# Kernel tuning notes

Measured on AMD Instinct MI355X. Metric: run time of the kernel, lower is better.

Reference implementation:

```python
import jax, jax.numpy as jnp
import numpy as np

EPS_BN = 1e-5
EPS_LN = 1e-5

def _gelu(x):
    return jax.nn.gelu(x, approximate=False)  # torch nn.GELU default is erf-based

def _conv(x, w, b, stride):
    y = jax.lax.conv_general_dilated(x, w, (stride, stride), 'VALID',
                                     dimension_numbers=('NCHW', 'OIHW', 'NCHW'))
    return y + b[None, :, None, None]

def _bn_train(x, g, b):
    # training-mode BatchNorm2d: batch statistics over (N,H,W), biased variance
    m = x.mean(axis=(0, 2, 3), keepdims=True)
    v = ((x - m) ** 2).mean(axis=(0, 2, 3), keepdims=True)
    return g[None, :, None, None] * (x - m) * jax.lax.rsqrt(v + EPS_BN) + b[None, :, None, None]

def _ln(x, g, b):
    m = x.mean(-1, keepdims=True)
    v = ((x - m) ** 2).mean(-1, keepdims=True)
    return g * (x - m) * jax.lax.rsqrt(v + EPS_LN) + b

def setup_inputs() -> dict:
    key = jax.random.key(0)
    ks = jax.random.split(key, 16)
    B, E, D, H = 1024, 8, 256, 512
    cnn_out = 128 * 14 * 16  # 28672
    s = 0.02
    inp = {
        'x': jax.random.normal(ks[0], (B, 4, 144, 160), jnp.float32),
        'conv1_w': jax.random.normal(ks[1], (32, 4, 8, 8), jnp.float32) * s,
        'conv1_b': jnp.zeros((32,), jnp.float32),
        'bn1_g': jnp.ones((32,), jnp.float32), 'bn1_b': jnp.zeros((32,), jnp.float32),
        'conv2_w': jax.random.normal(ks[2], (64, 32, 4, 4), jnp.float32) * s,
        'conv2_b': jnp.zeros((64,), jnp.float32),
        'bn2_g': jnp.ones((64,), jnp.float32), 'bn2_b': jnp.zeros((64,), jnp.float32),
        'conv3_w': jax.random.normal(ks[3], (128, 64, 3, 3), jnp.float32) * s,
        'conv3_b': jnp.zeros((128,), jnp.float32),
        'bn3_g': jnp.ones((128,), jnp.float32), 'bn3_b': jnp.zeros((128,), jnp.float32),
        'proj_w': jax.random.normal(ks[4], (D, cnn_out), jnp.float32) * 0.005,
        'proj_b': jnp.zeros((D,), jnp.float32),
        'ln_g': jnp.ones((D,), jnp.float32), 'ln_b': jnp.zeros((D,), jnp.float32),
        'router_w': jax.random.normal(ks[5], (E, D), jnp.float32) * 0.01,
        'expert_bias': jnp.zeros((E,), jnp.float32),
        'ew1': jax.random.normal(ks[6], (E, H, D), jnp.float32) * s,
        'eb1': jnp.zeros((E, H), jnp.float32),
        'ew2': jax.random.normal(ks[7], (E, D, H), jnp.float32) * s,
        'eb2': jnp.zeros((E, D), jnp.float32),
        'sw1': jax.random.normal(ks[8], (D, D), jnp.float32) * s,  # shared expert hidden = 512//2 = 256
        'sb1': jnp.zeros((D,), jnp.float32),
        'sw2': jax.random.normal(ks[9], (D, D), jnp.float32) * s,
        'sb2': jnp.zeros((D,), jnp.float32),
        'moe_ln_g': jnp.ones((D,), jnp.float32), 'moe_ln_b': jnp.zeros((D,), jnp.float32),
    }
    return inp

def reference(x, conv1_w, conv1_b, bn1_g, bn1_b, conv2_w, conv2_b, bn2_g, bn2_b,
              conv3_w, conv3_b, bn3_g, bn3_b, proj_w, proj_b, ln_g, ln_b,
              router_w, expert_bias, ew1, eb1, ew2, eb2, sw1, sb1, sw2, sb2,
              moe_ln_g, moe_ln_b):
    B = x.shape[0]
    E = router_w.shape[0]
    top_k = 2
    # conv backbone
    h = _gelu(_bn_train(_conv(x, conv1_w, conv1_b, 4), bn1_g, bn1_b))
    h = _gelu(_bn_train(_conv(h, conv2_w, conv2_b, 2), bn2_g, bn2_b))
    h = _gelu(_bn_train(_conv(h, conv3_w, conv3_b, 1), bn3_g, bn3_b))
    h = h.reshape(B, -1)  # [B, 128*14*16]
    # projection
    h = _gelu(_ln(h @ proj_w.T + proj_b, ln_g, ln_b))  # [B, 256]
    # router (eval: no noise)
    logits = h @ router_w.T + expert_bias          # [B, E]
    probs = jax.nn.softmax(logits, axis=-1)
    wts, idx = jax.lax.top_k(probs, top_k)          # [B, k]
    wts = wts / (wts.sum(-1, keepdims=True) + 1e-8)
    # dense expert compute, sparse combine (same math as masked dispatch loop)
    hid = _gelu(jnp.einsum('bd,ehd->beh', h, ew1) + eb1)   # [B, E, 512]
    eout = jnp.einsum('beh,edh->bed', hid, ew2) + eb2       # [B, E, 256]
    combine = jnp.zeros((B, E), h.dtype).at[jnp.arange(B)[:, None], idx].add(wts)
    out = jnp.einsum('be,bed->bd', combine, eout)
    # shared expert
    shared = _gelu(h @ sw1.T + sb1) @ sw2.T + sb2
    out = out + 0.5 * shared
    # aux losses
    pm = probs.mean(0)
    lb_loss = ((pm - 1.0 / E) ** 2).sum() * E
    z_loss = (logits ** 2).mean() * 0.001
    out = _ln(out, moe_ln_g, moe_ln_b)
    return out, lb_loss, z_loss
```

## Files before the change

kernel.cpp:

```cpp
#include <hip/hip_runtime.h>
#include <hip/hip_bf16.h>
#include <math.h>

typedef unsigned short u16;
typedef unsigned int u32;
typedef __attribute__((ext_vector_type(8))) short bf16x8;
typedef __attribute__((ext_vector_type(4))) float f32x4;

#define DEV __device__ __forceinline__

DEV float gelu_f(float x) { return 0.5f * x * (1.0f + erff(x * 0.70710678118654752f)); }
DEV u16 f2bf(float f) { u32 u = __builtin_bit_cast(u32, f); u = (u + 0x7FFFu + ((u >> 16) & 1u)) >> 16; return (u16)u; }
DEV float bf2f(u16 h) { return __builtin_bit_cast(float, (u32)h << 16); }
DEV u32 fbits(float f) { return __builtin_bit_cast(u32, f); }
DEV float ubits(u32 u) { return __builtin_bit_cast(float, u); }
DEV u32 psplit(float v) {
  u32 u = fbits(v);
  float lo = v - ubits(u & 0xFFFF0000u);
  return (u >> 16) | (fbits(lo) & 0xFFFF0000u);
}
DEV float punp(u32 p) { return ubits(p << 16) + ubits(p & 0xFFFF0000u); }
DEV f32x4 mfma3(bf16x8 ah, bf16x8 al, bf16x8 bh, bf16x8 bl, f32x4 c) {
  c = __builtin_amdgcn_mfma_f32_16x16x32_bf16(al, bh, c, 0, 0, 0);
  c = __builtin_amdgcn_mfma_f32_16x16x32_bf16(ah, bl, c, 0, 0, 0);
  c = __builtin_amdgcn_mfma_f32_16x16x32_bf16(ah, bh, c, 0, 0, 0);
  return c;
}

__global__ void k_zero(float* p, int n) {
  int i = blockIdx.x * blockDim.x + threadIdx.x;
  if (i < n) p[i] = 0.f;
}

__global__ void k_wprep1(const float* __restrict__ w, u16* __restrict__ wh, u16* __restrict__ wl) {
  int idx = blockIdx.x * 256 + threadIdx.x; if (idx >= 8192) return;
  int j = idx & 7, lane = (idx >> 3) & 63, s = (idx >> 9) & 7, oct = idx >> 12;
  int oc = oct * 16 + (lane & 15);
  int kl = ((lane >> 4) << 3) + j;
  int kw = kl >> 2, c = kl & 3, kh = s;
  float v = w[((oc * 4 + c) * 8 + kh) * 8 + kw];
  u16 h = f2bf(v); wh[idx] = h; wl[idx] = f2bf(v - bf2f(h));
}
__global__ void k_wprep2(const float* __restrict__ w, u16* __restrict__ wh, u16* __restrict__ wl) {
  int idx = blockIdx.x * 256 + threadIdx.x; if (idx >= 32768) return;
  int j = idx & 7, lane = (idx >> 3) & 63, s = (idx >> 9) & 15, oct = idx >> 13;
  int oc = oct * 16 + (lane & 15);
  int k = s * 32 + ((lane >> 4) << 3) + j;
  int kh = k >> 7, kw = (k >> 5) & 3, c = k & 31;
  float v = w[((oc * 32 + c) * 4 + kh) * 4 + kw];
  u16 h = f2bf(v); wh[idx] = h; wl[idx] = f2bf(v - bf2f(h));
}
__global__ void k_wprep3(const float* __restrict__ w, u16* __restrict__ wh, u16* __restrict__ wl) {
  int idx = blockIdx.x * 256 + threadIdx.x; if (idx >= 73728) return;
  int j = idx & 7, lane = (idx >> 3) & 63, rest = idx >> 9;
  int s = rest % 18, oct = rest / 18;
  int oc = oct * 16 + (lane & 15);
  int k = s * 32 + ((lane >> 4) << 3) + j;
  int kh = k / 192, r = k - kh * 192;
  int kw = r >> 6, c = r & 63;
  float v = w[((oc * 64 + c) * 3 + kh) * 3 + kw];
  u16 h = f2bf(v); wh[idx] = h; wl[idx] = f2bf(v - bf2f(h));
}
__global__ __launch_bounds__(256) void k_wprepP(const float* __restrict__ w,
    u16* __restrict__ wh, u16* __restrict__ wl)
{
  __shared__ float tile[16][4][225];
  int q = blockIdx.x, oct = blockIdx.y, tid = threadIdx.x;
  for (int i = tid; i < 3584; i += 256) {
    int n = i / 224, rem = i % 224, e = rem / 56, f4 = rem % 56;
    float4 v = *(const float4*)(w + (long)(oct * 16 + n) * 28672 + (4 * q + e) * 224 + f4 * 4);
    tile[n][e][f4 * 4 + 0] = v.x; tile[n][e][f4 * 4 + 1] = v.y;
    tile[n][e][f4 * 4 + 2] = v.z; tile[n][e][f4 * 4 + 3] = v.w;
  }
  __syncthreads();
  int g = (q >> 1) & 3, j0 = 4 * (q & 1), sgb = q >> 3;
  for (int o = tid; o < 3584; o += 256) {
    int pix = o >> 4, ln = o & 15;
    u16 hs[4], ls[4];
#pragma unroll
    for (int e = 0; e < 4; ++e) {
      float v = tile[ln][e][pix];
      u16 h = f2bf(v); hs[e] = h; ls[e] = f2bf(v - bf2f(h));
    }
    long base = (((long)oct * 896 + pix * 4 + sgb) * 64 + g * 16 + ln) * 8 + j0;
    *(uint2*)(wh + base) = make_uint2((u32)hs[0] | ((u32)hs[1] << 16), (u32)hs[2] | ((u32)hs[3] << 16));
    *(uint2*)(wl + base) = make_uint2((u32)ls[0] | ((u32)ls[1] << 16), (u32)ls[2] | ((u32)ls[3] << 16));
  }
}
__global__ void k_wprepG(const float* __restrict__ w, u16* __restrict__ wf,
                         int N, int K, long total)
{
  long idx = (long)blockIdx.x * 256 + threadIdx.x; if (idx >= total) return;
  int j = (int)(idx & 7); int lane = (int)((idx >> 3) & 63); long rest = idx >> 9;
  int kn = K >> 5;
  int s = (int)(rest % kn); long rest2 = rest / kn;
  int noct = N >> 4;
  int oct = (int)(rest2 % noct); int z = (int)(rest2 / noct);
  int n = oct * 16 + (lane & 15);
  int k = s * 32 + ((lane >> 4) << 3) + j;
  wf[idx] = f2bf(w[((long)z * N + n) * K + k]);
}

__global__ __launch_bounds__(256, 3) void k_conv1m(const float* __restrict__ x,
    const u16* __restrict__ wfh, const u16* __restrict__ wfl,
    const float* __restrict__ bias, u32* __restrict__ y1p, float* __restrict__ sums)
{
  __shared__ __align__(16) u16 sin0[12800], sin1[12800];
  __shared__ float bs1[32], bs2[32];
  int ohp = blockIdx.x, b = blockIdx.y, tid = threadIdx.x;
  int row0 = ohp * 16;
  if (tid < 32) { bs1[tid] = 0.f; bs2[tid] = 0.f; }
  for (int i = tid; i < 1600; i += 256) {
    int cp = i / 800, rem = i - cp * 800, r = rem / 40, q = rem - r * 40;
    int grow = row0 + r;
    float4 v0 = make_float4(0.f, 0.f, 0.f, 0.f), v1 = v0;
    if (grow < 144) {
      long base = ((long)b * 4 + 2 * cp) * 23040 + (long)grow * 160 + q * 4;
      v0 = *(const float4*)(x + base);
      v1 = *(const float4*)(x + base + 23040);
    }
    const float* a0 = (const float*)&v0;
    const float* a1 = (const float*)&v1;
#pragma unroll
    for (int m = 0; m < 4; ++m) {
      float f0 = a0[m], f1 = a1[m];
      u32 u0 = fbits(f0), u1 = fbits(f1);
      u32 hh = (u0 >> 16) | (u1 & 0xFFFF0000u);
      float l0 = f0 - ubits(u0 & 0xFFFF0000u);
      float l1 = f1 - ubits(u1 & 0xFFFF0000u);
      u32 ll = (fbits(l0) >> 16) | (fbits(l1) & 0xFFFF0000u);
      int col = q * 4 + m;
      int idx = r * 320 + col * 2 + cp;
      idx ^= ((col >> 4) & 3) << 2;
      ((u32*)sin0)[idx] = hh;
      ((u32*)sin1)[idx] = ll;
    }
  }
  __syncthreads();
  int w = tid >> 6, lane = tid & 63, g = lane >> 4, ln = lane & 15;
  int ohls[3], owcs[3];
#pragma unroll
  for (int jj = 0; jj < 3; ++jj) {
    int j = w + 4 * jj;
    ohls[jj] = j / 3;
    int owc = (j % 3) * 16 + ln; if (owc > 38) owc = 38;
    owcs[jj] = owc;
  }
  f32x4 z4 = {0.f, 0.f, 0.f, 0.f};
  f32x4 acc[3][2];
#pragma unroll
  for (int jj = 0; jj < 3; ++jj) { acc[jj][0] = z4; acc[jj][1] = z4; }
#pragma unroll
  for (int kh = 0; kh < 8; ++kh) {
    bf16x8 bh0 = *(const bf16x8*)&wfh[kh * 512 + lane * 8];
    bf16x8 bl0 = *(const bf16x8*)&wfl[kh * 512 + lane * 8];
    bf16x8 bh1 = *(const bf16x8*)&wfh[4096 + kh * 512 + lane * 8];
    bf16x8 bl1 = *(const bf16x8*)&wfl[4096 + kh * 512 + lane * 8];
#pragma unroll
    for (int jj = 0; jj < 3; ++jj) {
      int col = owcs[jj] * 4 + g * 2;
      int off = (4 * ohls[jj] + kh) * 640 + col * 4;
      off ^= ((col >> 4) & 3) << 3;
      bf16x8 ah = *(const bf16x8*)&sin0[off];
      bf16x8 al = *(const bf16x8*)&sin1[off];
      acc[jj][0] = mfma3(ah, al, bh0, bl0, acc[jj][0]);
      acc[jj][1] = mfma3(ah, al, bh1, bl1, acc[jj][1]);
    }
  }
  float s1[2] = {0.f, 0.f}, s2[2] = {0.f, 0.f};
#pragma unroll
  for (int jj = 0; jj < 3; ++jj) {
    int j = w + 4 * jj;
    int ohl = j / 3, owt = j % 3;
    int oh = 4 * ohp + ohl;
    if (oh >= 35) continue;
#pragma unroll
    for (int oct = 0; oct < 2; ++oct) {
      int oc = oct * 16 + ln;
      float bv = bias[oc];
#pragma unroll
      for (int r = 0; r < 4; ++r) {
        int owo = owt * 16 + g * 4 + r;
        if (owo < 39) {
          long oi = ((long)b * 1365 + oh * 39 + owo) * 32 + oc;
          float v = acc[jj][oct][r] + bv;
          y1p[oi] = psplit(v);
          s1[oct] += v; s2[oct] += v * v;
        }
      }
    }
  }
#pragma unroll
  for (int o = 16; o <= 32; o <<= 1) {
    s1[0] += __shfl_xor(s1[0], o); s1[1] += __shfl_xor(s1[1], o);
    s2[0] += __shfl_xor(s2[0], o); s2[1] += __shfl_xor(s2[1], o);
  }
  if (g == 0) {
    atomicAdd(&bs1[ln], s1[0]); atomicAdd(&bs1[16 + ln], s1[1]);
    atomicAdd(&bs2[ln], s2[0]); atomicAdd(&bs2[16 + ln], s2[1]);
  }
  __syncthreads();
  if (tid < 32) {
    atomicAdd(&sums[tid], bs1[tid]);
    atomicAdd(&sums[32 + tid], bs2[tid]);
  }
}

__global__ __launch_bounds__(256, 3) void k_conv2m(const u32* __restrict__ y1p,
    const u16* __restrict__ wfh, const u16* __restrict__ wfl,
    const float* __restrict__ scale, const float* __restrict__ shift,
    const float* __restrict__ bias, u32* __restrict__ y2p, float* __restrict__ sums)
{
  __shared__ __align__(16) u16 sin0[12480], sin1[12480];
  __shared__ float sc[32], shf[32];
  __shared__ float bs1[64], bs2[64];
  int ohq = blockIdx.x, b = blockIdx.y, tid = threadIdx.x;
  if (tid < 32) { sc[tid] = scale[tid]; shf[tid] = shift[tid]; }
  if (tid < 64) { bs1[tid] = 0.f; bs2[tid] = 0.f; }
  __syncthreads();
  long sb = ((long)b * 1365 + (long)ohq * 312) * 32;
  const uint4* srcP = (const uint4*)(y1p + sb);
  for (int i = tid; i < 3120; i += 256) {
    uint4 p4 = srcP[i];
    int cb = (i & 7) * 4;
    u32 hw[2], lw[2];
    u32 pe[4] = { p4.x, p4.y, p4.z, p4.w };
#pragma unroll
    for (int half = 0; half < 2; ++half) {
      float va = punp(pe[half * 2 + 0]);
      float vb = punp(pe[half * 2 + 1]);
      float aa = gelu_f(va * sc[cb + half * 2 + 0] + shf[cb + half * 2 + 0]);
      float ab = gelu_f(vb * sc[cb + half * 2 + 1] + shf[cb + half * 2 + 1]);
      u32 ua = fbits(aa), ub = fbits(ab);
      float la = aa - ubits(ua & 0xFFFF0000u);
      float lb = ab - ubits(ub & 0xFFFF0000u);
      hw[half] = (ua >> 16) | (ub & 0xFFFF0000u);
      lw[half] = (fbits(la) >> 16) | (fbits(lb) & 0xFFFF0000u);
    }
    int iw = i ^ (((i >> 4) & 7) << 1);
    ((uint2*)sin0)[iw] = make_uint2(hw[0], hw[1]);
    ((uint2*)sin1)[iw] = make_uint2(lw[0], lw[1]);
  }
  __syncthreads();
  int w = tid >> 6, lane = tid & 63, g = lane >> 4, ln = lane & 15;
  int oct = w;
  int rowb[5], colb[5];
#pragma unroll
  for (int j = 0; j < 5; ++j) {
    int p = j * 16 + ln; if (p > 71) p = 71;
    int ohl = p / 18, ow = p - 18 * ohl;
    rowb[j] = 2 * ohl; colb[j] = 2 * ow;
  }
  f32x4 z4 = {0.f, 0.f, 0.f, 0.f};
  f32x4 acc[5];
#pragma unroll
  for (int j = 0; j < 5; ++j) acc[j] = z4;
#pragma unroll
  for (int s = 0; s < 16; ++s) {
    int kh = s >> 2, kw = s & 3;
    bf16x8 bh = *(const bf16x8*)&wfh[oct * 8192 + s * 512 + lane * 8];
    bf16x8 bl = *(const bf16x8*)&wfl[oct * 8192 + s * 512 + lane * 8];
#pragma unroll
    for (int j = 0; j < 5; ++j) {
      int colpix = (rowb[j] + kh) * 39 + colb[j] + kw;
      int off = colpix * 32 + g * 8;
      off ^= ((colpix >> 1) & 7) << 3;
      bf16x8 ah = *(const bf16x8*)&sin0[off];
      bf16x8 al = *(const bf16x8*)&sin1[off];
      acc[j] = mfma3(ah, al, bh, bl, acc[j]);
    }
  }
  int oc = oct * 16 + ln;
  float bv = bias[oc];
  float s1 = 0.f, s2 = 0.f;
#pragma unroll
  for (int j = 0; j < 5; ++j) {
#pragma unroll
    for (int r = 0; r < 4; ++r) {
      int po = j * 16 + g * 4 + r;
      if (po < 72) {
        long oi = ((long)b * 288 + (long)ohq * 72 + po) * 64 + oc;
        float v = acc[j][r] + bv;
        y2p[oi] = psplit(v);
        s1 += v; s2 += v * v;
      }
    }
  }
#pragma unroll
  for (int o = 16; o <= 32; o <<= 1) { s1 += __shfl_xor(s1, o); s2 += __shfl_xor(s2, o); }
  if (g == 0) { atomicAdd(&bs1[oc], s1); atomicAdd(&bs2[oc], s2); }
  __syncthreads();
  if (tid < 64) {
    atomicAdd(&sums[tid], bs1[tid]);
    atomicAdd(&sums[64 + tid], bs2[tid]);
  }
}

__global__ __launch_bounds__(256, 3) void k_conv3m(const u32* __restrict__ y2p,
    const u16* __restrict__ wfh, const u16* __restrict__ wfl,
    const float* __restrict__ scale, const float* __restrict__ shift,
    const float* __restrict__ bias, u32* __restrict__ y3p, float* __restrict__ sums)
{
  __shared__ __align__(16) u16 sin0[10368], sin1[10368];
  __shared__ float sc[64], shf[64];
  __shared__ float bs1[128], bs2[128];
  int hh = blockIdx.x, b = blockIdx.y, tid = threadIdx.x;
  if (tid < 64) { sc[tid] = scale[tid]; shf[tid] = shift[tid]; }
  if (tid < 128) { bs1[tid] = 0.f; bs2[tid] = 0.f; }
  __syncthreads();
  long sb = ((long)b * 288 + (long)hh * 126) * 64;
  const uint4* srcP = (const uint4*)(y2p + sb);
  for (int i = tid; i < 2592; i += 256) {
    uint4 p4 = srcP[i];
    int cb = (i & 15) * 4;
    u32 hw[2], lw[2];
    u32 pe[4] = { p4.x, p4.y, p4.z, p4.w };
#pragma unroll
    for (int half = 0; half < 2; ++half) {
      float va = punp(pe[half * 2 + 0]);
      float vb = punp(pe[half * 2 + 1]);
      float aa = gelu_f(va * sc[cb + half * 2 + 0] + shf[cb + half * 2 + 0]);
      float ab = gelu_f(vb * sc[cb + half * 2 + 1] + shf[cb + half * 2 + 1]);
      u32 ua = fbits(aa), ub = fbits(ab);
      float la = aa - ubits(ua & 0xFFFF0000u);
      float lb = ab - ubits(ub & 0xFFFF0000u);
      hw[half] = (ua >> 16) | (ub & 0xFFFF0000u);
      lw[half] = (fbits(la) >> 16) | (fbits(lb) & 0xFFFF0000u);
    }
    int iw = i ^ (((i >> 4) & 7) << 1);
    ((uint2*)sin0)[iw] = make_uint2(hw[0], hw[1]);
    ((uint2*)sin1)[iw] = make_uint2(lw[0], lw[1]);
  }
  __syncthreads();
  int w = tid >> 6, lane = tid & 63, g = lane >> 4, ln = lane & 15;
  int oct0 = w * 2;
  f32x4 z4 = {0.f, 0.f, 0.f, 0.f};
  f32x4 acc[7][2];
#pragma unroll
  for (int j = 0; j < 7; ++j) { acc[j][0] = z4; acc[j][1] = z4; }
#pragma unroll 6
  for (int s = 0; s < 18; ++s) {
    const int kh = s / 6, rm = s % 6;
    const int kw = rm >> 1, ch = rm & 1;
    bf16x8 bh0 = *(const bf16x8*)&wfh[oct0 * 9216 + s * 512 + lane * 8];
    bf16x8 bl0 = *(const bf16x8*)&wfl[oct0 * 9216 + s * 512 + lane * 8];
    bf16x8 bh1 = *(const bf16x8*)&wfh[(oct0 + 1) * 9216 + s * 512 + lane * 8];
    bf16x8 bl1 = *(const bf16x8*)&wfl[(oct0 + 1) * 9216 + s * 512 + lane * 8];
#pragma unroll
    for (int j = 0; j < 7; ++j) {
      int colpix = (j + kh) * 18 + ln + kw;
      int off = colpix * 64 + ch * 32 + g * 8;
      off ^= (colpix & 7) << 3;
      bf16x8 ah = *(const bf16x8*)&sin0[off];
      bf16x8 al = *(const bf16x8*)&sin1[off];
      acc[j][0] = mfma3(ah, al, bh0, bl0, acc[j][0]);
      acc[j][1] = mfma3(ah, al, bh1, bl1, acc[j][1]);
    }
  }
  float s1[2] = {0.f, 0.f}, s2[2] = {0.f, 0.f};
#pragma unroll
  for (int j = 0; j < 7; ++j) {
#pragma unroll
    for (int o2 = 0; o2 < 2; ++o2) {
      int oc = (oct0 + o2) * 16 + ln;
      float bv = bias[oc];
#pragma unroll
      for (int r = 0; r < 4; ++r) {
        int owo = g * 4 + r;
        long oi = ((long)b * 224 + (hh * 7 + j) * 16 + owo) * 128 + oc;
        float v = acc[j][o2][r] + bv;
        y3p[oi] = psplit(v);
        s1[o2] += v; s2[o2] += v * v;
      }
    }
  }
#pragma unroll
  for (int o = 16; o <= 32; o <<= 1) {
    s1[0] += __shfl_xor(s1[0], o); s1[1] += __shfl_xor(s1[1], o);
    s2[0] += __shfl_xor(s2[0], o); s2[1] += __shfl_xor(s2[1], o);
  }
  if (g == 0) {
    atomicAdd(&bs1[oct0 * 16 + ln], s1[0]); atomicAdd(&bs1[(oct0 + 1) * 16 + ln], s1[1]);
    atomicAdd(&bs2[oct0 * 16 + ln], s2[0]); atomicAdd(&bs2[(oct0 + 1) * 16 + ln], s2[1]);
  }
  __syncthreads();
  if (tid < 128) {
    atomicAdd(&sums[tid], bs1[tid]);
    atomicAdd(&sums[128 + tid], bs2[tid]);
  }
}

__global__ void k_bn_finalize(const float* __restrict__ sums, const float* __restrict__ g,
    const float* __restrict__ b, float* __restrict__ scale, float* __restrict__ shift,
    int C, float invN)
{
  int c = threadIdx.x;
  if (c < C) {
    float m = sums[c] * invN;
    float var = sums[C + c] * invN - m * m;
    float sc = g[c] * rsqrtf(var + 1e-5f);
    scale[c] = sc;
    shift[c] = b[c] - m * sc;
  }
}

__global__ __launch_bounds__(256, 2) void k_projm(const u32* __restrict__ y3p,
    const u16* __restrict__ bh_g, const u16* __restrict__ bl_g,
    const float* __restrict__ scale, const float* __restrict__ shift,
    float* __restrict__ part)
{
  __shared__ __align__(16) u16 Ah[2048], Al[2048];
  __shared__ __align__(16) u16 Bh[8192], Bl[8192];
  __shared__ float sc3[128], sh3[128];
  int m0 = blockIdx.x * 64, by = blockIdx.y, tid = threadIdx.x;
  int w = tid >> 6, lane = tid & 63, g = lane >> 4, ln = lane & 15;
  if (tid < 128) { sc3[tid] = scale[tid]; sh3[tid] = shift[tid]; }
  f32x4 z4 = {0.f, 0.f, 0.f, 0.f};
  f32x4 acc[16];
#pragma unroll
  for (int o = 0; o < 16; ++o) acc[o] = z4;
  for (int ks = 0; ks < 28; ++ks) {
    __syncthreads();
    long k0 = ((long)by * 28 + ks) * 32;
    int cbase = (int)(k0 & 127);
    {
      for (int ii = 0; ii < 2; ++ii) {
        int i = tid + ii * 256;
        int row = i >> 3, q = i & 7;
        uint4 p4 = *((const uint4*)(y3p + (long)(m0 + row) * 28672 + k0) + q);
        u32 pe[4] = { p4.x, p4.y, p4.z, p4.w };
        int c0 = cbase + q * 4;
        u16 hs[4], ls[4];
#pragma unroll
        for (int j = 0; j < 4; ++j) {
          float v = punp(pe[j]);
          float a = gelu_f(v * sc3[c0 + j] + sh3[c0 + j]);
          u32 ua = fbits(a);
          float la = a - ubits(ua & 0xFFFF0000u);
          hs[j] = (u16)(ua >> 16);
          ls[j] = (u16)(fbits(la) >> 16);
        }
        ((uint2*)Ah)[i] = make_uint2((u32)hs[0] | ((u32)hs[1] << 16), (u32)hs[2] | ((u32)hs[3] << 16));
        ((uint2*)Al)[i] = make_uint2((u32)ls[0] | ((u32)ls[1] << 16), (u32)ls[2] | ((u32)ls[3] << 16));
      }
    }
    int ksg = by * 28 + ks;
#pragma unroll
    for (int ii = 0; ii < 8; ++ii) {
      int i = tid + ii * 256;
      int arr = i >> 10, idx = i & 1023, oct = idx >> 6, r2 = idx & 63;
      const u16* src = arr ? bl_g : bh_g;
      u16* dst = arr ? Bl : Bh;
      ((uint4*)dst)[idx] = *((const uint4*)(src + ((long)oct * 896 + ksg) * 512) + r2);
    }
    __syncthreads();
    bf16x8 a_h = *(const bf16x8*)&Ah[(w * 16 + ln) * 32 + g * 8];
    bf16x8 a_l = *(const bf16x8*)&Al[(w * 16 + ln) * 32 + g * 8];
#pragma unroll
    for (int oct = 0; oct < 16; ++oct) {
      bf16x8 bh = *(const bf16x8*)&Bh[oct * 512 + lane * 8];
      bf16x8 bl = *(const bf16x8*)&Bl[oct * 512 + lane * 8];
      acc[oct] = mfma3(a_h, a_l, bh, bl, acc[oct]);
    }
  }
#pragma unroll
  for (int oct = 0; oct < 16; ++oct) {
    int oc = oct * 16 + ln;
#pragma unroll
    for (int r = 0; r < 4; ++r) {
      int tok = m0 + w * 16 + g * 4 + r;
      part[((long)by * 1024 + tok) * 256 + oc] = acc[oct][r];
    }
  }
}

__global__ __launch_bounds__(256) void k_lnred(const float* __restrict__ part,
    const float* __restrict__ pb, const float* __restrict__ g, const float* __restrict__ be,
    float* __restrict__ h, u16* __restrict__ hb)
{
  int b = blockIdx.x, d = threadIdx.x;
  float s = pb[d];
#pragma unroll
  for (int ks = 0; ks < 32; ++ks) s += part[((long)ks * 1024 + b) * 256 + d];
  __shared__ float red[4];
  float t = s;
  for (int o = 32; o; o >>= 1) t += __shfl_xor(t, o);
  if ((d & 63) == 0) red[d >> 6] = t;
  __syncthreads();
  float mean = (red[0] + red[1] + red[2] + red[3]) * (1.f / 256.f);
  __syncthreads();
  float dv = s - mean;
  t = dv * dv;
  for (int o = 32; o; o >>= 1) t += __shfl_xor(t, o);
  if ((d & 63) == 0) red[d >> 6] = t;
  __syncthreads();
  float var = (red[0] + red[1] + red[2] + red[3]) * (1.f / 256.f);
  float hv = gelu_f(g[d] * dv * rsqrtf(var + 1e-5f) + be[d]);
  h[b * 256 + d] = hv;
  hb[b * 256 + d] = f2bf(hv);
}

__global__ __launch_bounds__(256, 2) void k_gemmb(const u16* __restrict__ A, long aZ, int K,
    const u16* __restrict__ Bf, int noct_tot,
    const float* __restrict__ bias, int biasZ,
    void* __restrict__ C, long cZ, int ldc, int outbf, int act)
{
  __shared__ __align__(16) u16 As[2048];
  __shared__ __align__(16) u16 Bs[8192];
  int m0 = blockIdx.x * 64, nb = blockIdx.y, z = blockIdx.z, tid = threadIdx.x;
  int w = tid >> 6, lane = tid & 63, g = lane >> 4, ln = lane & 15;
  const u16* Az = A + (long)z * aZ;
  int kn = K >> 5;
  f32x4 z4 = {0.f, 0.f, 0.f, 0.f};
  f32x4 acc[16];
#pragma unroll
  for (int o = 0; o < 16; ++o) acc[o] = z4;
  for (int ks = 0; ks < kn; ++ks) {
    __syncthreads();
    {
      int row = tid >> 2, q = tid & 3;
      ((uint4*)As)[tid] = *((const uint4*)(Az + (long)(m0 + row) * K + ks * 32) + q);
    }
#pragma unroll
    for (int ii = 0; ii < 4; ++ii) {
      int i = tid + ii * 256;
      int oct = i >> 6, r2 = i & 63;
      const u16* src = Bf + (((long)z * noct_tot + nb * 16 + oct) * kn + ks) * 512;
      ((uint4*)Bs)[i] = ((const uint4*)src)[r2];
    }
    __syncthreads();
    bf16x8 a = *(const bf16x8*)&As[(w * 16 + ln) * 32 + g * 8];
#pragma unroll
    for (int oct = 0; oct < 16; ++oct) {
      bf16x8 bb = *(const bf16x8*)&Bs[oct * 512 + lane * 8];
      acc[oct] = __builtin_amdgcn_mfma_f32_16x16x32_bf16(a, bb, acc[oct], 0, 0, 0);
    }
  }
#pragma unroll
  for (int oct = 0; oct < 16; ++oct) {
    int n = nb * 256 + oct * 16 + ln;
    float bv = bias[z * biasZ + n];
#pragma unroll
    for (int r = 0; r < 4; ++r) {
      int tok = m0 + w * 16 + g * 4 + r;
      float v = acc[oct][r] + bv;
      if (act) v = gelu_f(v);
      long off = (long)z * cZ + (long)tok * ldc + n;
      if (outbf) ((u16*)C)[off] = f2bf(v);
      else ((float*)C)[off] = v;
    }
  }
}

__global__ __launch_bounds__(64) void k_router(const float* __restrict__ h,
    const float* __restrict__ rw, const float* __restrict__ eb,
    float* __restrict__ wts, int* __restrict__ idx,
    float* __restrict__ pm_sum, float* __restrict__ z_sum)
{
  int b = blockIdx.x, lane = threadIdx.x;
  float4 hv = *(const float4*)(h + b * 256 + lane * 4);
  float logit[8];
#pragma unroll
  for (int e = 0; e < 8; ++e) {
    float4 wv = *(const float4*)(rw + e * 256 + lane * 4);
    float p = hv.x * wv.x + hv.y * wv.y + hv.z * wv.z + hv.w * wv.w;
    for (int o = 32; o; o >>= 1) p += __shfl_xor(p, o);
    logit[e] = p + eb[e];
  }
  float mx = logit[0];
#pragma unroll
  for (int e = 1; e < 8; ++e) mx = fmaxf(mx, logit[e]);
  float pr[8]; float se = 0.f;
#pragma unroll
  for (int e = 0; e < 8; ++e) { pr[e] = expf(logit[e] - mx); se += pr[e]; }
  float inv = 1.f / se;
#pragma unroll
  for (int e = 0; e < 8; ++e) pr[e] *= inv;
  int i0 = 0; float v0 = pr[0];
#pragma unroll
  for (int e = 1; e < 8; ++e) if (pr[e] > v0) { v0 = pr[e]; i0 = e; }
  int i1 = -1; float v1 = -1.f;
#pragma unroll
  for (int e = 0; e < 8; ++e) if (e != i0 && pr[e] > v1) { v1 = pr[e]; i1 = e; }
  if (lane == 0) {
    float ssum = v0 + v1 + 1e-8f;
    wts[2 * b] = v0 / ssum; wts[2 * b + 1] = v1 / ssum;
    idx[2 * b] = i0; idx[2 * b + 1] = i1;
    float zz = 0.f;
#pragma unroll
    for (int e = 0; e < 8; ++e) zz += logit[e] * logit[e];
    atomicAdd(z_sum, zz);
  }
  if (lane < 8) atomicAdd(&pm_sum[lane], pr[lane]);
}

__global__ __launch_bounds__(256) void k_combine_ln(const float* __restrict__ eout,
    const float* __restrict__ sharedB, const float* __restrict__ wts, const int* __restrict__ idx,
    const float* __restrict__ g, const float* __restrict__ bb, float* __restrict__ out)
{
  int b = blockIdx.x, d = threadIdx.x;
  float w0 = wts[2 * b], w1 = wts[2 * b + 1];
  int i0 = idx[2 * b], i1 = idx[2 * b + 1];
  float val = w0 * eout[(long)i0 * 262144 + b * 256 + d]
            + w1 * eout[(long)i1 * 262144 + b * 256 + d]
            + 0.5f * sharedB[b * 256 + d];
  __shared__ float red[4];
  float s = val;
  for (int o = 32; o; o >>= 1) s += __shfl_xor(s, o);
  if ((d & 63) == 0) red[d >> 6] = s;
  __syncthreads();
  float mean = (red[0] + red[1] + red[2] + red[3]) * (1.f / 256.f);
  __syncthreads();
  float dv = val - mean;
  s = dv * dv;
  for (int o = 32; o; o >>= 1) s += __shfl_xor(s, o);
  if ((d & 63) == 0) red[d >> 6] = s;
  __syncthreads();
  float var = (red[0] + red[1] + red[2] + red[3]) * (1.f / 256.f);
  out[b * 256 + d] = g[d] * dv * rsqrtf(var + 1e-5f) + bb[d];
}

__global__ void k_losses(const float* __restrict__ pm_sum, const float* __restrict__ z_sum,
                         float* __restrict__ out)
{
  if (threadIdx.x == 0 && blockIdx.x == 0) {
    float lb = 0.f;
    for (int e = 0; e < 8; ++e) {
      float pm = pm_sum[e] * (1.f / 1024.f);
      float dd = pm - 0.125f;
      lb += dd * dd;
    }
    out[262144] = lb * 8.f;
    out[262145] = z_sum[0] * (1.f / 8192.f) * 0.001f;
  }
}

extern "C" void kernel_launch(void* const* d_in, const int* in_sizes, int n_in,
                              void* d_out, int out_size, void* d_ws, size_t ws_size,
                              hipStream_t stream)
{
  const float* x     = (const float*)d_in[0];
  const float* c1w   = (const float*)d_in[1];
  const float* c1b   = (const float*)d_in[2];
  const float* bn1g  = (const float*)d_in[3];
  const float* bn1b  = (const float*)d_in[4];
  const float* c2w   = (const float*)d_in[5];
  const float* c2b   = (const float*)d_in[6];
  const float* bn2g  = (const float*)d_in[7];
  const float* bn2b  = (const float*)d_in[8];
  const float* c3w   = (const float*)d_in[9];
  const float* c3b   = (const float*)d_in[10];
  const float* bn3g  = (const float*)d_in[11];
  const float* bn3b  = (const float*)d_in[12];
  const float* projw = (const float*)d_in[13];
  const float* projb = (const float*)d_in[14];
  const float* lng   = (const float*)d_in[15];
  const float* lnb   = (const float*)d_in[16];
  const float* rw    = (const float*)d_in[17];
  const float* ebias = (const float*)d_in[18];
  const float* ew1   = (const float*)d_in[19];
  const float* eb1   = (const float*)d_in[20];
  const float* ew2   = (const float*)d_in[21];
  const float* eb2   = (const float*)d_in[22];
  const float* sw1   = (const float*)d_in[23];
  const float* sb1   = (const float*)d_in[24];
  const float* sw2   = (const float*)d_in[25];
  const float* sb2   = (const float*)d_in[26];
  const float* mlng  = (const float*)d_in[27];
  const float* mlnb  = (const float*)d_in[28];
  float* out = (float*)d_out;

  char* W = (char*)d_ws;
  u32* y1p = (u32*)(W + 0);
  u32* y2p = (u32*)(W + 178913280L);
  u32* y3p = (u32*)(W + 0);
  u16* wfph = (u16*)(W + 254410752L);
  u16* wfpl = (u16*)(W + 269090816L);
  u16* wf1h = (u16*)(W + 283770880L);
  u16* wf1l = (u16*)(W + 283787264L);
  u16* wf2h = (u16*)(W + 283803648L);
  u16* wf2l = (u16*)(W + 283869184L);
  u16* wf3h = (u16*)(W + 283934720L);
  u16* wf3l = (u16*)(W + 284082176L);
  float* stats = (float*)(W + 284229632L);
  float* wtsb  = (float*)(W + 284233728L);
  int*   idxb  = (int*)(W + 284241920L);
  float* hbuf  = (float*)(W + 284250112L);
  float* shB   = (float*)(W + 286347264L);
  float* part  = (float*)(W + 178913280L);
  u16* hid     = (u16*)(W + 212467712L);
  u16* ewf1    = (u16*)(W + 220856320L);
  u16* ewf2    = (u16*)(W + 222953472L);
  u16* swf1    = (u16*)(W + 225050624L);
  u16* swf2    = (u16*)(W + 225181696L);
  float* eoutB = (float*)(W + 225312768L);
  u16* hbufb   = (u16*)(W + 233701376L);
  u16* sh1b    = (u16*)(W + 234225664L);

  float* sums1 = stats;        float* scale1 = stats + 512; float* shift1 = stats + 544;
  float* sums2 = stats + 64;   float* scale2 = stats + 576; float* shift2 = stats + 640;
  float* sums3 = stats + 192;  float* scale3 = stats + 704; float* shift3 = stats + 832;
  float* pm    = stats + 448;  float* zsum   = stats + 456;

  dim3 blk(256);
  k_zero<<<dim3(2), blk, 0, stream>>>(stats, 512);
  k_wprep1<<<dim3(32), blk, 0, stream>>>(c1w, wf1h, wf1l);
  k_wprep2<<<dim3(128), blk, 0, stream>>>(c2w, wf2h, wf2l);
  k_wprep3<<<dim3(288), blk, 0, stream>>>(c3w, wf3h, wf3l);
  k_wprepP<<<dim3(32, 16), blk, 0, stream>>>(projw, wfph, wfpl);

  k_conv1m<<<dim3(9, 1024), blk, 0, stream>>>(x, wf1h, wf1l, c1b, y1p, sums1);
  k_bn_finalize<<<1, 32, 0, stream>>>(sums1, bn1g, bn1b, scale1, shift1, 32, 1.f / 1397760.f);

  k_conv2m<<<dim3(4, 1024), blk, 0, stream>>>(y1p, wf2h, wf2l, scale1, shift1, c2b, y2p, sums2);
  k_bn_finalize<<<1, 64, 0, stream>>>(sums2, bn2g, bn2b, scale2, shift2, 64, 1.f / 294912.f);

  k_conv3m<<<dim3(2, 1024), blk, 0, stream>>>(y2p, wf3h, wf3l, scale2, shift2, c3b, y3p, sums3);
  k_bn_finalize<<<1, 128, 0, stream>>>(sums3, bn3g, bn3b, scale3, shift3, 128, 1.f / 229376.f);

  k_wprepG<<<dim3(4096), blk, 0, stream>>>(ew1, ewf1, 512, 256, 1048576L);
  k_wprepG<<<dim3(4096), blk, 0, stream>>>(ew2, ewf2, 256, 512, 1048576L);
  k_wprepG<<<dim3(256), blk, 0, stream>>>(sw1, swf1, 256, 256, 65536L);
  k_wprepG<<<dim3(256), blk, 0, stream>>>(sw2, swf2, 256, 256, 65536L);

  k_projm<<<dim3(16, 32), blk, 0, stream>>>(y3p, wfph, wfpl, scale3, shift3, part);
  k_lnred<<<dim3(1024), blk, 0, stream>>>(part, projb, lng, lnb, hbuf, hbufb);

  k_router<<<dim3(1024), dim3(64), 0, stream>>>(hbuf, rw, ebias, wtsb, idxb, pm, zsum);

  k_gemmb<<<dim3(16, 2, 8), blk, 0, stream>>>(hbufb, 0L, 256, ewf1, 32, eb1, 512,
                                              (void*)hid, 524288L, 512, 1, 1);
  k_gemmb<<<dim3(16, 1, 8), blk, 0, stream>>>(hid, 524288L, 512, ewf2, 16, eb2, 256,
                                              (void*)eoutB, 262144L, 256, 0, 0);
  k_gemmb<<<dim3(16, 1, 1), blk, 0, stream>>>(hbufb, 0L, 256, swf1, 16, sb1, 0,
                                              (void*)sh1b, 0L, 256, 1, 1);
  k_gemmb<<<dim3(16, 1, 1), blk, 0, stream>>>(sh1b, 0L, 256, swf2, 16, sb2, 0,
                                              (void*)shB, 0L, 256, 0, 0);

  k_combine_ln<<<dim3(1024), blk, 0, stream>>>(eoutB, shB, wtsb, idxb, mlng, mlnb, out);
  k_losses<<<1, 64, 0, stream>>>(pm, zsum, out);
}
```

Baseline: 807.8 us.

## Shard BN stat atomics across 8 buckets and double projection M-tile

The conv kernels now spread their per-channel sum and sum-of-squares atomics over 8 buckets chosen by batch index, and bn_finalize adds the buckets back together. This is meant to reduce contention on a single set of global atomic addresses. Separately, the projection GEMM tile grows from 64 to 128 tokens per block, so each wave computes two 16-row subtiles and reuses every loaded weight fragment twice. That halves the weight traffic through LDS, at the cost of a doubled accumulator count that adds register pressure and only 256 blocks in the grid.

```diff
diff --git a/kernel.cpp b/kernel.cpp
--- a/kernel.cpp
+++ b/kernel.cpp
@@ -200,9 +200,10 @@
     atomicAdd(&bs2[ln], s2[0]); atomicAdd(&bs2[16 + ln], s2[1]);
   }
   __syncthreads();
+  int bkt = b & 7;
   if (tid < 32) {
-    atomicAdd(&sums[tid], bs1[tid]);
-    atomicAdd(&sums[32 + tid], bs2[tid]);
+    atomicAdd(&sums[bkt * 64 + tid], bs1[tid]);
+    atomicAdd(&sums[bkt * 64 + 32 + tid], bs2[tid]);
   }
 }
 
@@ -290,9 +291,10 @@
   for (int o = 16; o <= 32; o <<= 1) { s1 += __shfl_xor(s1, o); s2 += __shfl_xor(s2, o); }
   if (g == 0) { atomicAdd(&bs1[oc], s1); atomicAdd(&bs2[oc], s2); }
   __syncthreads();
+  int bkt = b & 7;
   if (tid < 64) {
-    atomicAdd(&sums[tid], bs1[tid]);
-    atomicAdd(&sums[64 + tid], bs2[tid]);
+    atomicAdd(&sums[bkt * 128 + tid], bs1[tid]);
+    atomicAdd(&sums[bkt * 128 + 64 + tid], bs2[tid]);
   }
 }
 
@@ -384,9 +386,10 @@
     atomicAdd(&bs2[oct0 * 16 + ln], s2[0]); atomicAdd(&bs2[(oct0 + 1) * 16 + ln], s2[1]);
   }
   __syncthreads();
+  int bkt = b & 7;
   if (tid < 128) {
-    atomicAdd(&sums[tid], bs1[tid]);
-    atomicAdd(&sums[128 + tid], bs2[tid]);
+    atomicAdd(&sums[bkt * 256 + tid], bs1[tid]);
+    atomicAdd(&sums[bkt * 256 + 128 + tid], bs2[tid]);
   }
 }
 
@@ -396,8 +399,14 @@
 {
   int c = threadIdx.x;
   if (c < C) {
-    float m = sums[c] * invN;
-    float var = sums[C + c] * invN - m * m;
+    float s1 = 0.f, s2 = 0.f;
+#pragma unroll
+    for (int k = 0; k < 8; ++k) {
+      s1 += sums[k * 2 * C + c];
+      s2 += sums[k * 2 * C + C + c];
+    }
+    float m = s1 * invN;
+    float var = s2 * invN - m * m;
     float sc = g[c] * rsqrtf(var + 1e-5f);
     scale[c] = sc;
     shift[c] = b[c] - m * sc;
@@ -409,40 +418,41 @@
     const float* __restrict__ scale, const float* __restrict__ shift,
     float* __restrict__ part)
 {
-  __shared__ __align__(16) u16 Ah[2048], Al[2048];
+  __shared__ __align__(16) u16 Ah[4096], Al[4096];
   __shared__ __align__(16) u16 Bh[8192], Bl[8192];
   __shared__ float sc3[128], sh3[128];
-  int m0 = blockIdx.x * 64, by = blockIdx.y, tid = threadIdx.x;
+  int m0 = blockIdx.x * 128, by = blockIdx.y, tid = threadIdx.x;
   int w = tid >> 6, lane = tid & 63, g = lane >> 4, ln = lane & 15;
   if (tid < 128) { sc3[tid] = scale[tid]; sh3[tid] = shift[tid]; }
   f32x4 z4 = {0.f, 0.f, 0.f, 0.f};
-  f32x4 acc[16];
-#pragma unroll
-  for (int o = 0; o < 16; ++o) acc[o] = z4;
+  f32x4 acc[2][16];
+#pragma unroll
+  for (int p = 0; p < 2; ++p)
+#pragma unroll
+    for (int o = 0; o < 16; ++o) acc[p][o] = z4;
   for (int ks = 0; ks < 28; ++ks) {
     __syncthreads();
     long k0 = ((long)by * 28 + ks) * 32;
     int cbase = (int)(k0 & 127);
-    {
-      for (int ii = 0; ii < 2; ++ii) {
-        int i = tid + ii * 256;
-        int row = i >> 3, q = i & 7;
-        uint4 p4 = *((const uint4*)(y3p + (long)(m0 + row) * 28672 + k0) + q);
-        u32 pe[4] = { p4.x, p4.y, p4.z, p4.w };
-        int c0 = cbase + q * 4;
-        u16 hs[4], ls[4];
-#pragma unroll
-        for (int j = 0; j < 4; ++j) {
-          float v = punp(pe[j]);
-          float a = gelu_f(v * sc3[c0 + j] + sh3[c0 + j]);
-          u32 ua = fbits(a);
-          float la = a - ubits(ua & 0xFFFF0000u);
-          hs[j] = (u16)(ua >> 16);
-          ls[j] = (u16)(fbits(la) >> 16);
-        }
-        ((uint2*)Ah)[i] = make_uint2((u32)hs[0] | ((u32)hs[1] << 16), (u32)hs[2] | ((u32)hs[3] << 16));
-        ((uint2*)Al)[i] = make_uint2((u32)ls[0] | ((u32)ls[1] << 16), (u32)ls[2] | ((u32)ls[3] << 16));
+#pragma unroll
+    for (int ii = 0; ii < 4; ++ii) {
+      int i = tid + ii * 256;
+      int row = i >> 3, q = i & 7;
+      uint4 p4 = *((const uint4*)(y3p + (long)(m0 + row) * 28672 + k0) + q);
+      u32 pe[4] = { p4.x, p4.y, p4.z, p4.w };
+      int c0 = cbase + q * 4;
+      u16 hs[4], ls[4];
+#pragma unroll
+      for (int j = 0; j < 4; ++j) {
+        float v = punp(pe[j]);
+        float a = gelu_f(v * sc3[c0 + j] + sh3[c0 + j]);
+        u32 ua = fbits(a);
+        float la = a - ubits(ua & 0xFFFF0000u);
+        hs[j] = (u16)(ua >> 16);
+        ls[j] = (u16)(fbits(la) >> 16);
       }
+      ((uint2*)Ah)[i] = make_uint2((u32)hs[0] | ((u32)hs[1] << 16), (u32)hs[2] | ((u32)hs[3] << 16));
+      ((uint2*)Al)[i] = make_uint2((u32)ls[0] | ((u32)ls[1] << 16), (u32)ls[2] | ((u32)ls[3] << 16));
     }
     int ksg = by * 28 + ks;
 #pragma unroll
@@ -454,24 +464,33 @@
       ((uint4*)dst)[idx] = *((const uint4*)(src + ((long)oct * 896 + ksg) * 512) + r2);
     }
     __syncthreads();
-    bf16x8 a_h = *(const bf16x8*)&Ah[(w * 16 + ln) * 32 + g * 8];
-    bf16x8 a_l = *(const bf16x8*)&Al[(w * 16 + ln) * 32 + g * 8];
+    bf16x8 a_h[2], a_l[2];
+#pragma unroll
+    for (int pt = 0; pt < 2; ++pt) {
+      int off = ((2 * w + pt) * 16 + ln) * 32 + g * 8;
+      a_h[pt] = *(const bf16x8*)&Ah[off];
+      a_l[pt] = *(const bf16x8*)&Al[off];
+    }
 #pragma unroll
     for (int oct = 0; oct < 16; ++oct) {
       bf16x8 bh = *(const bf16x8*)&Bh[oct * 512 + lane * 8];
       bf16x8 bl = *(const bf16x8*)&Bl[oct * 512 + lane * 8];
-      acc[oct] = mfma3(a_h, a_l, bh, bl, acc[oct]);
-    }
-  }
-#pragma unroll
-  for (int oct = 0; oct < 16; ++oct) {
-    int oc = oct * 16 + ln;
-#pragma unroll
-    for (int r = 0; r < 4; ++r) {
-      int tok = m0 + w * 16 + g * 4 + r;
-      part[((long)by * 1024 + tok) * 256 + oc] = acc[oct][r];
-    }
-  }
+#pragma unroll
+      for (int pt = 0; pt < 2; ++pt)
+        acc[pt][oct] = mfma3(a_h[pt], a_l[pt], bh, bl, acc[pt][oct]);
+    }
+  }
+#pragma unroll
+  for (int pt = 0; pt < 2; ++pt)
+#pragma unroll
+    for (int oct = 0; oct < 16; ++oct) {
+      int oc = oct * 16 + ln;
+#pragma unroll
+      for (int r = 0; r < 4; ++r) {
+        int tok = m0 + (2 * w + pt) * 16 + g * 4 + r;
+        part[((long)by * 1024 + tok) * 256 + oc] = acc[pt][oct][r];
+      }
+    }
 }
 
 __global__ __launch_bounds__(256) void k_lnred(const float* __restrict__ part,
@@ -683,10 +702,10 @@
   u16* wf3h = (u16*)(W + 283934720L);
   u16* wf3l = (u16*)(W + 284082176L);
   float* stats = (float*)(W + 284229632L);
-  float* wtsb  = (float*)(W + 284233728L);
-  int*   idxb  = (int*)(W + 284241920L);
-  float* hbuf  = (float*)(W + 284250112L);
-  float* shB   = (float*)(W + 286347264L);
+  float* wtsb  = (float*)(W + 284246016L);
+  int*   idxb  = (int*)(W + 284254208L);
+  float* hbuf  = (float*)(W + 284262400L);
+  float* shB   = (float*)(W + 286359552L);
   float* part  = (float*)(W + 178913280L);
   u16* hid     = (u16*)(W + 212467712L);
   u16* ewf1    = (u16*)(W + 220856320L);
@@ -697,13 +716,16 @@
   u16* hbufb   = (u16*)(W + 233701376L);
   u16* sh1b    = (u16*)(W + 234225664L);
 
-  float* sums1 = stats;        float* scale1 = stats + 512; float* shift1 = stats + 544;
-  float* sums2 = stats + 64;   float* scale2 = stats + 576; float* shift2 = stats + 640;
-  float* sums3 = stats + 192;  float* scale3 = stats + 704; float* shift3 = stats + 832;
-  float* pm    = stats + 448;  float* zsum   = stats + 456;
+  float* sums1 = stats;
+  float* sums2 = stats + 512;
+  float* sums3 = stats + 1536;
+  float* scale1 = stats + 3584; float* shift1 = stats + 3616;
+  float* scale2 = stats + 3648; float* shift2 = stats + 3712;
+  float* scale3 = stats + 3776; float* shift3 = stats + 3904;
+  float* pm    = stats + 4032;  float* zsum  = stats + 4040;
 
   dim3 blk(256);
-  k_zero<<<dim3(2), blk, 0, stream>>>(stats, 512);
+  k_zero<<<dim3(16), blk, 0, stream>>>(stats, 4096);
   k_wprep1<<<dim3(32), blk, 0, stream>>>(c1w, wf1h, wf1l);
   k_wprep2<<<dim3(128), blk, 0, stream>>>(c2w, wf2h, wf2l);
   k_wprep3<<<dim3(288), blk, 0, stream>>>(c3w, wf3h, wf3l);
@@ -723,7 +745,7 @@
   k_wprepG<<<dim3(256), blk, 0, stream>>>(sw1, swf1, 256, 256, 65536L);
   k_wprepG<<<dim3(256), blk, 0, stream>>>(sw2, swf2, 256, 256, 65536L);
 
-  k_projm<<<dim3(16, 32), blk, 0, stream>>>(y3p, wfph, wfpl, scale3, shift3, part);
+  k_projm<<<dim3(8, 32), blk, 0, stream>>>(y3p, wfph, wfpl, scale3, shift3, part);
   k_lnred<<<dim3(1024), blk, 0, stream>>>(part, projb, lng, lnb, hbuf, hbufb);
 
   k_router<<<dim3(1024), dim3(64), 0, stream>>>(hbuf, rw, ebias, wtsb, idxb, pm, zsum);
```

After: 773.9 us. 4.2% less time.
